# Kernel optimization log

Hardware: AMD Instinct MI355X
Metric: run time of the kernel (lower is better)

Reference implementation:

```python
import jax, jax.numpy as jnp
import numpy as np

N = 100000
E = 3200000
F_IN = 27
H1, C1 = 8, 8
H2, C2 = 1, 2
NEG_SLOPE = 0.2


def gat_conv(x, src, dst, W, a_src, a_dst, b, heads, ch, n_nodes):
    # x: [N, F_in]; src/dst: [E'] (self-loops already appended)
    h = (x @ W).reshape(n_nodes, heads, ch)            # [N, H, C]
    alpha_src = jnp.sum(h * a_src, axis=-1)            # [N, H]
    alpha_dst = jnp.sum(h * a_dst, axis=-1)            # [N, H]
    e = jax.nn.leaky_relu(alpha_src[src] + alpha_dst[dst], NEG_SLOPE)  # [E', H]
    m = jax.ops.segment_max(e, dst, num_segments=n_nodes)             # [N, H]
    ex = jnp.exp(e - m[dst])
    denom = jax.ops.segment_sum(ex, dst, num_segments=n_nodes)        # [N, H]
    alpha = ex / denom[dst]                                           # [E', H]
    out = jax.ops.segment_sum(h[src] * alpha[:, :, None], dst, num_segments=n_nodes)
    return out.reshape(n_nodes, heads * ch) + b


def setup_inputs() -> dict:
    key = jax.random.key(0)
    ks = jax.random.split(key, 10)
    x = jax.random.normal(ks[0], (N, F_IN), dtype=jnp.float32)
    edge_index = jax.random.randint(ks[1], (2, E), 0, N, dtype=jnp.int64)
    s1 = 1.0 / np.sqrt(F_IN)
    s2 = 1.0 / np.sqrt(H1 * C1)
    W1 = jax.random.uniform(ks[2], (F_IN, H1 * C1), jnp.float32, -s1, s1)
    a_src1 = jax.random.uniform(ks[3], (H1, C1), jnp.float32, -s1, s1)
    a_dst1 = jax.random.uniform(ks[4], (H1, C1), jnp.float32, -s1, s1)
    b1 = jnp.zeros((H1 * C1,), jnp.float32)
    W2 = jax.random.uniform(ks[5], (H1 * C1, H2 * C2), jnp.float32, -s2, s2)
    a_src2 = jax.random.uniform(ks[6], (H2, C2), jnp.float32, -s2, s2)
    a_dst2 = jax.random.uniform(ks[7], (H2, C2), jnp.float32, -s2, s2)
    b2 = jnp.zeros((H2 * C2,), jnp.float32)
    return {"x": x, "edge_index": edge_index, "W1": W1, "a_src1": a_src1,
            "a_dst1": a_dst1, "b1": b1, "W2": W2, "a_src2": a_src2,
            "a_dst2": a_dst2, "b2": b2}


def reference(x, edge_index, W1, a_src1, a_dst1, b1, W2, a_src2, a_dst2, b2):
    # eval mode: dropouts are identity. PyG GATConv adds self-loops by default.
    loop = jnp.arange(N, dtype=edge_index.dtype)
    src = jnp.concatenate([edge_index[0], loop])
    dst = jnp.concatenate([edge_index[1], loop])
    h = jax.nn.elu(gat_conv(x, src, dst, W1, a_src1, a_dst1, b1, H1, C1, N))
    out = gat_conv(h, src, dst, W2, a_src2, a_dst2, b2, H2, C2, N)
    return jax.nn.log_softmax(out, axis=1)
```

## Files before the change

kernel.cpp:

```cpp
#include <hip/hip_runtime.h>
#include <hip/hip_fp16.h>
#include <math.h>

#define NN 100000
#define EE 3200000
#define ET (EE + NN)

#define H1n 8
#define C1n 8
#define F1n 64
#define FINn 27
#define NEG 0.2f

#define NPB 128
#define NB 782
#define STRIDE 5120
#define TILE 4096
#define ABLK 256
#define WIN (STRIDE + NPB)

typedef float floatx2 __attribute__((ext_vector_type(2)));

static __device__ __forceinline__ float lrelu(float v) {
    return v > 0.f ? v : NEG * v;
}

__global__ __launch_bounds__(ABLK) void k_binA(const int* __restrict__ ei,
                                               int* __restrict__ tail,
                                               int* __restrict__ recs) {
    __shared__ int hist[NB];
    __shared__ int lofs[NB];
    __shared__ int cur[NB];
    __shared__ int gpos[NB];
    __shared__ int sorted[TILE];
    __shared__ unsigned short sbkt[TILE];
    __shared__ int part[ABLK];

    int tid = threadIdx.x;
    long long e0 = (long long)blockIdx.x * TILE;
    int cnt = (int)min((long long)TILE, (long long)EE - e0);

    for (int i = tid; i < NB; i += ABLK) hist[i] = 0;
    __syncthreads();

    int ss[TILE / ABLK], dd[TILE / ABLK];
    #pragma unroll
    for (int k = 0; k < TILE / ABLK; ++k) {
        int idx = k * ABLK + tid;
        if (idx < cnt) {
            ss[k] = ei[e0 + idx];
            dd[k] = ei[EE + e0 + idx];
            atomicAdd(&hist[dd[k] >> 7], 1);
        }
    }
    __syncthreads();
    {
        const int CH = (NB + ABLK - 1) / ABLK;
        int beg = tid * CH, end = min(beg + CH, NB);
        int s = 0;
        for (int i = beg; i < end; ++i) s += hist[i];
        part[tid] = s;
        __syncthreads();
        for (int off = 1; off < ABLK; off <<= 1) {
            int add = (tid >= off) ? part[tid - off] : 0;
            __syncthreads();
            part[tid] += add;
            __syncthreads();
        }
        int ex = (tid > 0) ? part[tid - 1] : 0;
        for (int i = beg; i < end; ++i) {
            lofs[i] = ex;
            cur[i] = ex;
            ex += hist[i];
        }
    }
    __syncthreads();
    #pragma unroll
    for (int k = 0; k < TILE / ABLK; ++k) {
        int idx = k * ABLK + tid;
        if (idx < cnt) {
            int b = dd[k] >> 7;
            int r = atomicAdd(&cur[b], 1);
            sorted[r] = ss[k] | ((dd[k] & (NPB - 1)) << 17);
            sbkt[r] = (unsigned short)b;
        }
    }
    __syncthreads();
    for (int i = tid; i < NB; i += ABLK) {
        int c = hist[i];
        if (c > 0) gpos[i] = atomicAdd(&tail[i], c);
    }
    __syncthreads();
    for (int t = tid; t < cnt; t += ABLK) {
        int b = sbkt[t];
        recs[(size_t)b * STRIDE + gpos[b] + (t - lofs[b])] = sorted[t];
    }
}

__global__ void k_bscan(const int* __restrict__ tail, int* __restrict__ bbase) {
    __shared__ int part[256];
    int tid = threadIdx.x;
    const int CH = (NB + 255) / 256;
    int beg = tid * CH, end = min(beg + CH, NB);
    int s = 0;
    for (int i = beg; i < end; ++i)
        s += tail[i] + min(NPB, NN - i * NPB);
    part[tid] = s;
    __syncthreads();
    for (int off = 1; off < 256; off <<= 1) {
        int add = (tid >= off) ? part[tid - off] : 0;
        __syncthreads();
        part[tid] += add;
        __syncthreads();
    }
    int ex = (tid > 0) ? part[tid - 1] : 0;
    for (int i = beg; i < end; ++i) {
        bbase[i] = ex;
        ex += tail[i] + min(NPB, NN - i * NPB);
    }
}

__global__ __launch_bounds__(128) void k_binB(const int* __restrict__ recs,
                                              const int* __restrict__ tail,
                                              const int* __restrict__ bbase,
                                              int* __restrict__ rowptr,
                                              int* __restrict__ csr) {
    __shared__ int hist[NPB];
    __shared__ int cur[NPB];
    __shared__ int window[WIN];
    __shared__ int wtot[2];

    int b = blockIdx.x;
    int tid = threadIdx.x;
    int node0 = b * NPB;
    int nodes = min(NPB, NN - node0);
    int cnt = tail[b];
    const int* rb = recs + (size_t)b * STRIDE;

    hist[tid] = 0;
    __syncthreads();
    for (int i = tid; i < cnt; i += 128) atomicAdd(&hist[rb[i] >> 17], 1);
    __syncthreads();
    int v = (tid < nodes) ? hist[tid] + 1 : 0;
    int inc = v;
    #pragma unroll
    for (int off = 1; off < 64; off <<= 1) {
        int t = __shfl_up(inc, off, 64);
        if ((tid & 63) >= off) inc += t;
    }
    if ((tid & 63) == 63) wtot[tid >> 6] = inc;
    __syncthreads();
    if (tid >= 64) inc += wtot[0];
    int T = wtot[0] + wtot[1];
    int ex = inc - v;
    int base = bbase[b];
    if (tid < nodes) {
        rowptr[node0 + tid] = base + ex;
        window[ex] = node0 + tid;
        cur[tid] = ex + 1;
    }
    if (b == NB - 1 && tid == 0) rowptr[NN] = base + T;
    __syncthreads();
    for (int i = tid; i < cnt; i += 128) {
        int r = rb[i];
        int p = atomicAdd(&cur[r >> 17], 1);
        window[p] = r & 0x1FFFF;
    }
    __syncthreads();
    for (int i = tid; i < T; i += 128) csr[base + i] = window[i];
}

__global__ __launch_bounds__(256) void k_h1(const float* __restrict__ x,
                                            const float* __restrict__ W1,
                                            const float* __restrict__ a_src1,
                                            const float* __restrict__ a_dst1,
                                            unsigned char* __restrict__ h1q,
                                            __half* __restrict__ as1h,
                                            float* __restrict__ ad1) {
    int gt = blockIdx.x * blockDim.x + threadIdx.x;
    int n = gt >> 6;
    if (n >= NN) return;
    int lane = threadIdx.x & 63;
    const float* xr = x + (size_t)n * FINn;
    float s = 0.f;
    #pragma unroll
    for (int k = 0; k < FINn; ++k) s = fmaf(xr[k], W1[k * F1n + lane], s);
    float s2 = __shfl_down(s, 1, 64);
    if (!(lane & 1)) {
        int pk = __builtin_amdgcn_cvt_pk_fp8_f32(s, s2, 0, false);
        ((unsigned short*)(h1q + (size_t)n * F1n))[lane >> 1] =
            (unsigned short)(pk & 0xFFFF);
    }
    float ps = s * a_src1[lane];
    float pd = s * a_dst1[lane];
    #pragma unroll
    for (int off = 1; off < 8; off <<= 1) {
        ps += __shfl_xor(ps, off, 64);
        pd += __shfl_xor(pd, off, 64);
    }
    if ((lane & 7) == 0) {
        int h = lane >> 3;
        as1h[n * H1n + h] = __float2half(ps);
        ad1[n * H1n + h] = pd;
    }
}

__global__ __launch_bounds__(256) void k_l1(const int* __restrict__ rowptr,
                                            const int* __restrict__ csr,
                                            const unsigned* __restrict__ h1q,
                                            const __half* __restrict__ as1h,
                                            const float* __restrict__ ad1,
                                            const float* __restrict__ b1,
                                            const float* __restrict__ W2,
                                            const float* __restrict__ a_src2,
                                            const float* __restrict__ a_dst2,
                                            uint2* __restrict__ rec2) {
    int gt = blockIdx.x * blockDim.x + threadIdx.x;
    int n = gt >> 6;
    if (n >= NN) return;
    int lane = threadIdx.x & 63;
    int e8 = lane >> 3;
    int hh = lane & 7;
    int q = lane >> 4;
    int c4 = lane & 15;
    float adh = ad1[(n << 3) + hh];
    int bpe = e8 << 2;
    int bpq = q << 2;
    int bpx = ((q << 3) + (c4 >> 1)) << 2;

    int beg = rowptr[n], end = rowptr[n + 1];
    float a0 = 0.f, a1 = 0.f, a2 = 0.f, a3 = 0.f, den = 0.f;

    for (int base = beg; base < end; base += 64) {
        int cnt = min(64, end - base);
        int sidx = (lane < cnt) ? csr[base + lane] : 0;
        for (int sb = 0; sb < cnt; sb += 8) {
            int sb4 = sb << 2;
            int s_sc = __builtin_amdgcn_ds_bpermute(sb4 + bpe, sidx);
            float A = __half2float(as1h[((unsigned)s_sc << 3) + hh]);
            float sc = A + adh;
            sc = fmaxf(sc, 0.2f * sc);
            float x = (sb + e8 < cnt) ? __expf(sc) : 0.f;
            den += x;
            int xi = __float_as_int(x);
            #pragma unroll
            for (int jj = 0; jj < 2; ++jj) {
                int s_a = __builtin_amdgcn_ds_bpermute(sb4 + (jj << 4) + bpq, sidx);
                int xr_ = __builtin_amdgcn_ds_bpermute((jj << 7) + bpx, xi);
                float xv = __int_as_float(xr_);
                unsigned dw = h1q[((unsigned)s_a << 4) + c4];
                floatx2 lo = __builtin_amdgcn_cvt_pk_f32_fp8((int)dw, false);
                floatx2 hi = __builtin_amdgcn_cvt_pk_f32_fp8((int)dw, true);
                a0 = fmaf(xv, lo.x, a0);
                a1 = fmaf(xv, lo.y, a1);
                a2 = fmaf(xv, hi.x, a2);
                a3 = fmaf(xv, hi.y, a3);
            }
        }
    }

    den += __shfl_xor(den, 8, 64);
    den += __shfl_xor(den, 16, 64);
    den += __shfl_xor(den, 32, 64);
    den = __int_as_float(
        __builtin_amdgcn_ds_bpermute((c4 >> 1) << 2, __float_as_int(den)));
    #pragma unroll
    for (int off = 16; off < 64; off <<= 1) {
        a0 += __shfl_xor(a0, off, 64);
        a1 += __shfl_xor(a1, off, 64);
        a2 += __shfl_xor(a2, off, 64);
        a3 += __shfl_xor(a3, off, 64);
    }
    float inv = 1.f / den;
    float v0 = a0 * inv + b1[c4 * 4 + 0];
    float v1 = a1 * inv + b1[c4 * 4 + 1];
    float v2 = a2 * inv + b1[c4 * 4 + 2];
    float v3 = a3 * inv + b1[c4 * 4 + 3];
    v0 = v0 > 0.f ? v0 : expm1f(v0);
    v1 = v1 > 0.f ? v1 : expm1f(v1);
    v2 = v2 > 0.f ? v2 : expm1f(v2);
    v3 = v3 > 0.f ? v3 : expm1f(v3);
    float p0 = v0 * W2[(c4 * 4 + 0) * 2 + 0] + v1 * W2[(c4 * 4 + 1) * 2 + 0] +
               v2 * W2[(c4 * 4 + 2) * 2 + 0] + v3 * W2[(c4 * 4 + 3) * 2 + 0];
    float p1 = v0 * W2[(c4 * 4 + 0) * 2 + 1] + v1 * W2[(c4 * 4 + 1) * 2 + 1] +
               v2 * W2[(c4 * 4 + 2) * 2 + 1] + v3 * W2[(c4 * 4 + 3) * 2 + 1];
    #pragma unroll
    for (int off = 1; off < 16; off <<= 1) {
        p0 += __shfl_xor(p0, off, 64);
        p1 += __shfl_xor(p1, off, 64);
    }
    if (lane == 0) {
        float as2 = p0 * a_src2[0] + p1 * a_src2[1];
        float ad2 = p0 * a_dst2[0] + p1 * a_dst2[1];
        __half2 lo2 = __floats2half2_rn(p0, p1);
        __half2 hi2 = __floats2half2_rn(as2, ad2);
        uint2 r;
        r.x = *(unsigned*)&lo2;
        r.y = *(unsigned*)&hi2;
        rec2[n] = r;
    }
}

__global__ __launch_bounds__(256) void k_l2(const int* __restrict__ rowptr,
                                            const int* __restrict__ csr,
                                            const uint2* __restrict__ rec2,
                                            const float* __restrict__ b2,
                                            float* __restrict__ out) {
    int gt = blockIdx.x * blockDim.x + threadIdx.x;
    int n = gt >> 6;
    if (n >= NN) return;
    int lane = threadIdx.x & 63;
    __half2 mysd = *(const __half2*)&rec2[n].y;
    float adv = __half2float(__high2half(mysd));
    int beg = rowptr[n], end = rowptr[n + 1];
    float den = 0.f, a0 = 0.f, a1 = 0.f;
    for (int i = beg + lane; i < end; i += 64) {
        int s = csr[i];
        uint2 rv = rec2[s];
        __half2 h01 = *(const __half2*)&rv.x;
        __half2 hsd = *(const __half2*)&rv.y;
        float e = lrelu(__half2float(__low2half(hsd)) + adv);
        float ex = __expf(e);
        den += ex;
        a0 = fmaf(ex, __half2float(__low2half(h01)), a0);
        a1 = fmaf(ex, __half2float(__high2half(h01)), a1);
    }
    #pragma unroll
    for (int off = 32; off > 0; off >>= 1) {
        den += __shfl_xor(den, off, 64);
        a0 += __shfl_xor(a0, off, 64);
        a1 += __shfl_xor(a1, off, 64);
    }
    if (lane == 0) {
        float v0 = a0 / den + b2[0];
        float v1 = a1 / den + b2[1];
        float mx = fmaxf(v0, v1);
        float ls = mx + logf(__expf(v0 - mx) + __expf(v1 - mx));
        out[n * 2 + 0] = v0 - ls;
        out[n * 2 + 1] = v1 - ls;
    }
}

extern "C" void kernel_launch(void* const* d_in, const int* in_sizes, int n_in,
                              void* d_out, int out_size, void* d_ws, size_t ws_size,
                              hipStream_t stream) {
    const float* x      = (const float*)d_in[0];
    const int*   ei     = (const int*)d_in[1];
    const float* W1     = (const float*)d_in[2];
    const float* a_src1 = (const float*)d_in[3];
    const float* a_dst1 = (const float*)d_in[4];
    const float* b1     = (const float*)d_in[5];
    const float* W2     = (const float*)d_in[6];
    const float* a_src2 = (const float*)d_in[7];
    const float* a_dst2 = (const float*)d_in[8];
    const float* b2     = (const float*)d_in[9];
    float* out = (float*)d_out;

    char* wsb = (char*)d_ws;
    size_t o = 0;
    uint2* rec2 = (uint2*)wsb;                   o += (size_t)NN * 8;
    #define ALLOC(name, type, count) type* name = (type*)(wsb + o); o += (size_t)(count) * 4;
    ALLOC(ad1,    float, NN * H1n)
    ALLOC(rowptr, int,   NN + 1)
    ALLOC(csr,    int,   ET)
    ALLOC(recs,   int,   (size_t)NB * STRIDE)
    ALLOC(tail,   int,   NB)
    ALLOC(bbase,  int,   NB)
    #undef ALLOC
    __half* as1h = (__half*)(wsb + o);               o += (size_t)NN * H1n * 2;
    unsigned char* h1q = (unsigned char*)(wsb + o);  o += (size_t)NN * F1n;

    const int B = 256;
    #define GRID(n) ((unsigned)(((long long)(n) + B - 1) / B))

    hipMemsetAsync(tail, 0, (size_t)NB * sizeof(int), stream);
    k_binA<<<(EE + TILE - 1) / TILE, ABLK, 0, stream>>>(ei, tail, recs);
    k_bscan<<<1, 256, 0, stream>>>(tail, bbase);
    k_binB<<<NB, 128, 0, stream>>>(recs, tail, bbase, rowptr, csr);

    k_h1<<<GRID((size_t)NN * 64), B, 0, stream>>>(x, W1, a_src1, a_dst1, h1q, as1h, ad1);

    k_l1<<<GRID((size_t)NN * 64), B, 0, stream>>>(rowptr, csr, (const unsigned*)h1q,
                                                  as1h, ad1, b1, W2, a_src2, a_dst2, rec2);

    k_l2<<<GRID((size_t)NN * 64), B, 0, stream>>>(rowptr, csr, rec2, b2, out);
    #undef GRID
}
```

Measured before the change: 233.6 us.

## Fuse bucket-local CSR build into both GAT aggregation kernels, drop global CSR

Removes the global scan and CSR-building kernels. Each of the two aggregation kernels now rebuilds the per-bucket adjacency of 128 nodes in shared memory from the binned records, then processes those nodes with 8 waves per block. This saves the global CSR and rowptr writes and reads plus two launches. In exchange the bucket-local sort is done twice, the grid shrinks to 782 blocks of 512 threads, and the large shared-memory window may limit occupancy.

```diff
diff --git a/kernel.cpp b/kernel.cpp
--- a/kernel.cpp
+++ b/kernel.cpp
@@ -18,6 +18,7 @@
 #define TILE 4096
 #define ABLK 256
 #define WIN (STRIDE + NPB)
+#define FBLK 512
 
 typedef float floatx2 __attribute__((ext_vector_type(2)));
 
@@ -95,79 +96,6 @@
         int b = sbkt[t];
         recs[(size_t)b * STRIDE + gpos[b] + (t - lofs[b])] = sorted[t];
     }
-}
-
-__global__ void k_bscan(const int* __restrict__ tail, int* __restrict__ bbase) {
-    __shared__ int part[256];
-    int tid = threadIdx.x;
-    const int CH = (NB + 255) / 256;
-    int beg = tid * CH, end = min(beg + CH, NB);
-    int s = 0;
-    for (int i = beg; i < end; ++i)
-        s += tail[i] + min(NPB, NN - i * NPB);
-    part[tid] = s;
-    __syncthreads();
-    for (int off = 1; off < 256; off <<= 1) {
-        int add = (tid >= off) ? part[tid - off] : 0;
-        __syncthreads();
-        part[tid] += add;
-        __syncthreads();
-    }
-    int ex = (tid > 0) ? part[tid - 1] : 0;
-    for (int i = beg; i < end; ++i) {
-        bbase[i] = ex;
-        ex += tail[i] + min(NPB, NN - i * NPB);
-    }
-}
-
-__global__ __launch_bounds__(128) void k_binB(const int* __restrict__ recs,
-                                              const int* __restrict__ tail,
-                                              const int* __restrict__ bbase,
-                                              int* __restrict__ rowptr,
-                                              int* __restrict__ csr) {
-    __shared__ int hist[NPB];
-    __shared__ int cur[NPB];
-    __shared__ int window[WIN];
-    __shared__ int wtot[2];
-
-    int b = blockIdx.x;
-    int tid = threadIdx.x;
-    int node0 = b * NPB;
-    int nodes = min(NPB, NN - node0);
-    int cnt = tail[b];
-    const int* rb = recs + (size_t)b * STRIDE;
-
-    hist[tid] = 0;
-    __syncthreads();
-    for (int i = tid; i < cnt; i += 128) atomicAdd(&hist[rb[i] >> 17], 1);
-    __syncthreads();
-    int v = (tid < nodes) ? hist[tid] + 1 : 0;
-    int inc = v;
-    #pragma unroll
-    for (int off = 1; off < 64; off <<= 1) {
-        int t = __shfl_up(inc, off, 64);
-        if ((tid & 63) >= off) inc += t;
-    }
-    if ((tid & 63) == 63) wtot[tid >> 6] = inc;
-    __syncthreads();
-    if (tid >= 64) inc += wtot[0];
-    int T = wtot[0] + wtot[1];
-    int ex = inc - v;
-    int base = bbase[b];
-    if (tid < nodes) {
-        rowptr[node0 + tid] = base + ex;
-        window[ex] = node0 + tid;
-        cur[tid] = ex + 1;
-    }
-    if (b == NB - 1 && tid == 0) rowptr[NN] = base + T;
-    __syncthreads();
-    for (int i = tid; i < cnt; i += 128) {
-        int r = rb[i];
-        int p = atomicAdd(&cur[r >> 17], 1);
-        window[p] = r & 0x1FFFF;
-    }
-    __syncthreads();
-    for (int i = tid; i < T; i += 128) csr[base + i] = window[i];
 }
 
 __global__ __launch_bounds__(256) void k_h1(const float* __restrict__ x,
@@ -205,139 +133,235 @@
     }
 }
 
-__global__ __launch_bounds__(256) void k_l1(const int* __restrict__ rowptr,
-                                            const int* __restrict__ csr,
-                                            const unsigned* __restrict__ h1q,
-                                            const __half* __restrict__ as1h,
-                                            const float* __restrict__ ad1,
-                                            const float* __restrict__ b1,
-                                            const float* __restrict__ W2,
-                                            const float* __restrict__ a_src2,
-                                            const float* __restrict__ a_dst2,
-                                            uint2* __restrict__ rec2) {
-    int gt = blockIdx.x * blockDim.x + threadIdx.x;
-    int n = gt >> 6;
-    if (n >= NN) return;
-    int lane = threadIdx.x & 63;
+__global__ __launch_bounds__(FBLK) void k_f1(const int* __restrict__ recs,
+                                             const int* __restrict__ tail,
+                                             const unsigned* __restrict__ h1q,
+                                             const __half* __restrict__ as1h,
+                                             const float* __restrict__ ad1,
+                                             const float* __restrict__ b1,
+                                             const float* __restrict__ W2,
+                                             const float* __restrict__ a_src2,
+                                             const float* __restrict__ a_dst2,
+                                             uint2* __restrict__ rec2) {
+    __shared__ int hist[NPB];
+    __shared__ int cur[NPB];
+    __shared__ int rloc[NPB + 1];
+    __shared__ int window[WIN];
+    __shared__ int wtot[2];
+
+    int b = blockIdx.x;
+    int tid = threadIdx.x;
+    int node0 = b * NPB;
+    int nodes = min(NPB, NN - node0);
+    int rcnt = tail[b];
+    const int* rb = recs + (size_t)b * STRIDE;
+
+    if (tid < NPB) hist[tid] = 0;
+    __syncthreads();
+    for (int i = tid; i < rcnt; i += FBLK) atomicAdd(&hist[rb[i] >> 17], 1);
+    __syncthreads();
+    int v = 0, inc = 0;
+    if (tid < NPB) {
+        v = (tid < nodes) ? hist[tid] + 1 : 0;
+        inc = v;
+        #pragma unroll
+        for (int off = 1; off < 64; off <<= 1) {
+            int t = __shfl_up(inc, off, 64);
+            if ((tid & 63) >= off) inc += t;
+        }
+        if ((tid & 63) == 63) wtot[tid >> 6] = inc;
+    }
+    __syncthreads();
+    if (tid < NPB) {
+        if (tid >= 64) inc += wtot[0];
+        int ex = inc - v;
+        if (tid < nodes) {
+            rloc[tid] = ex;
+            cur[tid] = ex + 1;
+            window[ex] = node0 + tid;
+        }
+    }
+    if (tid == 0) rloc[nodes] = wtot[0] + wtot[1];
+    __syncthreads();
+    for (int i = tid; i < rcnt; i += FBLK) {
+        int r = rb[i];
+        int p = atomicAdd(&cur[r >> 17], 1);
+        window[p] = r & 0x1FFFF;
+    }
+    __syncthreads();
+
+    int lane = tid & 63;
+    int wv = tid >> 6;
     int e8 = lane >> 3;
     int hh = lane & 7;
     int q = lane >> 4;
     int c4 = lane & 15;
-    float adh = ad1[(n << 3) + hh];
     int bpe = e8 << 2;
     int bpq = q << 2;
     int bpx = ((q << 3) + (c4 >> 1)) << 2;
 
-    int beg = rowptr[n], end = rowptr[n + 1];
-    float a0 = 0.f, a1 = 0.f, a2 = 0.f, a3 = 0.f, den = 0.f;
-
-    for (int base = beg; base < end; base += 64) {
-        int cnt = min(64, end - base);
-        int sidx = (lane < cnt) ? csr[base + lane] : 0;
-        for (int sb = 0; sb < cnt; sb += 8) {
-            int sb4 = sb << 2;
-            int s_sc = __builtin_amdgcn_ds_bpermute(sb4 + bpe, sidx);
-            float A = __half2float(as1h[((unsigned)s_sc << 3) + hh]);
-            float sc = A + adh;
-            sc = fmaxf(sc, 0.2f * sc);
-            float x = (sb + e8 < cnt) ? __expf(sc) : 0.f;
-            den += x;
-            int xi = __float_as_int(x);
-            #pragma unroll
-            for (int jj = 0; jj < 2; ++jj) {
-                int s_a = __builtin_amdgcn_ds_bpermute(sb4 + (jj << 4) + bpq, sidx);
-                int xr_ = __builtin_amdgcn_ds_bpermute((jj << 7) + bpx, xi);
-                float xv = __int_as_float(xr_);
-                unsigned dw = h1q[((unsigned)s_a << 4) + c4];
-                floatx2 lo = __builtin_amdgcn_cvt_pk_f32_fp8((int)dw, false);
-                floatx2 hi = __builtin_amdgcn_cvt_pk_f32_fp8((int)dw, true);
-                a0 = fmaf(xv, lo.x, a0);
-                a1 = fmaf(xv, lo.y, a1);
-                a2 = fmaf(xv, hi.x, a2);
-                a3 = fmaf(xv, hi.y, a3);
+    for (int ln = wv; ln < nodes; ln += FBLK / 64) {
+        int n = node0 + ln;
+        float adh = ad1[(n << 3) + hh];
+        int beg = rloc[ln], end = rloc[ln + 1];
+        float a0 = 0.f, a1 = 0.f, a2 = 0.f, a3 = 0.f, den = 0.f;
+
+        for (int base = beg; base < end; base += 64) {
+            int cnt = min(64, end - base);
+            int sidx = (lane < cnt) ? window[base + lane] : 0;
+            for (int sb = 0; sb < cnt; sb += 8) {
+                int sb4 = sb << 2;
+                int s_sc = __builtin_amdgcn_ds_bpermute(sb4 + bpe, sidx);
+                float A = __half2float(as1h[((unsigned)s_sc << 3) + hh]);
+                float sc = A + adh;
+                sc = fmaxf(sc, 0.2f * sc);
+                float x = (sb + e8 < cnt) ? __expf(sc) : 0.f;
+                den += x;
+                int xi = __float_as_int(x);
+                #pragma unroll
+                for (int jj = 0; jj < 2; ++jj) {
+                    int s_a = __builtin_amdgcn_ds_bpermute(sb4 + (jj << 4) + bpq, sidx);
+                    int xr_ = __builtin_amdgcn_ds_bpermute((jj << 7) + bpx, xi);
+                    float xv = __int_as_float(xr_);
+                    unsigned dw = h1q[((unsigned)s_a << 4) + c4];
+                    floatx2 lo = __builtin_amdgcn_cvt_pk_f32_fp8((int)dw, false);
+                    floatx2 hi = __builtin_amdgcn_cvt_pk_f32_fp8((int)dw, true);
+                    a0 = fmaf(xv, lo.x, a0);
+                    a1 = fmaf(xv, lo.y, a1);
+                    a2 = fmaf(xv, hi.x, a2);
+                    a3 = fmaf(xv, hi.y, a3);
+                }
             }
         }
-    }
-
-    den += __shfl_xor(den, 8, 64);
-    den += __shfl_xor(den, 16, 64);
-    den += __shfl_xor(den, 32, 64);
-    den = __int_as_float(
-        __builtin_amdgcn_ds_bpermute((c4 >> 1) << 2, __float_as_int(den)));
-    #pragma unroll
-    for (int off = 16; off < 64; off <<= 1) {
-        a0 += __shfl_xor(a0, off, 64);
-        a1 += __shfl_xor(a1, off, 64);
-        a2 += __shfl_xor(a2, off, 64);
-        a3 += __shfl_xor(a3, off, 64);
-    }
-    float inv = 1.f / den;
-    float v0 = a0 * inv + b1[c4 * 4 + 0];
-    float v1 = a1 * inv + b1[c4 * 4 + 1];
-    float v2 = a2 * inv + b1[c4 * 4 + 2];
-    float v3 = a3 * inv + b1[c4 * 4 + 3];
-    v0 = v0 > 0.f ? v0 : expm1f(v0);
-    v1 = v1 > 0.f ? v1 : expm1f(v1);
-    v2 = v2 > 0.f ? v2 : expm1f(v2);
-    v3 = v3 > 0.f ? v3 : expm1f(v3);
-    float p0 = v0 * W2[(c4 * 4 + 0) * 2 + 0] + v1 * W2[(c4 * 4 + 1) * 2 + 0] +
-               v2 * W2[(c4 * 4 + 2) * 2 + 0] + v3 * W2[(c4 * 4 + 3) * 2 + 0];
-    float p1 = v0 * W2[(c4 * 4 + 0) * 2 + 1] + v1 * W2[(c4 * 4 + 1) * 2 + 1] +
-               v2 * W2[(c4 * 4 + 2) * 2 + 1] + v3 * W2[(c4 * 4 + 3) * 2 + 1];
-    #pragma unroll
-    for (int off = 1; off < 16; off <<= 1) {
-        p0 += __shfl_xor(p0, off, 64);
-        p1 += __shfl_xor(p1, off, 64);
-    }
-    if (lane == 0) {
-        float as2 = p0 * a_src2[0] + p1 * a_src2[1];
-        float ad2 = p0 * a_dst2[0] + p1 * a_dst2[1];
-        __half2 lo2 = __floats2half2_rn(p0, p1);
-        __half2 hi2 = __floats2half2_rn(as2, ad2);
-        uint2 r;
-        r.x = *(unsigned*)&lo2;
-        r.y = *(unsigned*)&hi2;
-        rec2[n] = r;
-    }
-}
-
-__global__ __launch_bounds__(256) void k_l2(const int* __restrict__ rowptr,
-                                            const int* __restrict__ csr,
-                                            const uint2* __restrict__ rec2,
-                                            const float* __restrict__ b2,
-                                            float* __restrict__ out) {
-    int gt = blockIdx.x * blockDim.x + threadIdx.x;
-    int n = gt >> 6;
-    if (n >= NN) return;
-    int lane = threadIdx.x & 63;
-    __half2 mysd = *(const __half2*)&rec2[n].y;
-    float adv = __half2float(__high2half(mysd));
-    int beg = rowptr[n], end = rowptr[n + 1];
-    float den = 0.f, a0 = 0.f, a1 = 0.f;
-    for (int i = beg + lane; i < end; i += 64) {
-        int s = csr[i];
-        uint2 rv = rec2[s];
-        __half2 h01 = *(const __half2*)&rv.x;
-        __half2 hsd = *(const __half2*)&rv.y;
-        float e = lrelu(__half2float(__low2half(hsd)) + adv);
-        float ex = __expf(e);
-        den += ex;
-        a0 = fmaf(ex, __half2float(__low2half(h01)), a0);
-        a1 = fmaf(ex, __half2float(__high2half(h01)), a1);
-    }
-    #pragma unroll
-    for (int off = 32; off > 0; off >>= 1) {
-        den += __shfl_xor(den, off, 64);
-        a0 += __shfl_xor(a0, off, 64);
-        a1 += __shfl_xor(a1, off, 64);
-    }
-    if (lane == 0) {
-        float v0 = a0 / den + b2[0];
-        float v1 = a1 / den + b2[1];
-        float mx = fmaxf(v0, v1);
-        float ls = mx + logf(__expf(v0 - mx) + __expf(v1 - mx));
-        out[n * 2 + 0] = v0 - ls;
-        out[n * 2 + 1] = v1 - ls;
+
+        den += __shfl_xor(den, 8, 64);
+        den += __shfl_xor(den, 16, 64);
+        den += __shfl_xor(den, 32, 64);
+        den = __int_as_float(
+            __builtin_amdgcn_ds_bpermute((c4 >> 1) << 2, __float_as_int(den)));
+        #pragma unroll
+        for (int off = 16; off < 64; off <<= 1) {
+            a0 += __shfl_xor(a0, off, 64);
+            a1 += __shfl_xor(a1, off, 64);
+            a2 += __shfl_xor(a2, off, 64);
+            a3 += __shfl_xor(a3, off, 64);
+        }
+        float inv = 1.f / den;
+        float v0 = a0 * inv + b1[c4 * 4 + 0];
+        float v1 = a1 * inv + b1[c4 * 4 + 1];
+        float v2 = a2 * inv + b1[c4 * 4 + 2];
+        float v3 = a3 * inv + b1[c4 * 4 + 3];
+        v0 = v0 > 0.f ? v0 : expm1f(v0);
+        v1 = v1 > 0.f ? v1 : expm1f(v1);
+        v2 = v2 > 0.f ? v2 : expm1f(v2);
+        v3 = v3 > 0.f ? v3 : expm1f(v3);
+        float p0 = v0 * W2[(c4 * 4 + 0) * 2 + 0] + v1 * W2[(c4 * 4 + 1) * 2 + 0] +
+                   v2 * W2[(c4 * 4 + 2) * 2 + 0] + v3 * W2[(c4 * 4 + 3) * 2 + 0];
+        float p1 = v0 * W2[(c4 * 4 + 0) * 2 + 1] + v1 * W2[(c4 * 4 + 1) * 2 + 1] +
+                   v2 * W2[(c4 * 4 + 2) * 2 + 1] + v3 * W2[(c4 * 4 + 3) * 2 + 1];
+        #pragma unroll
+        for (int off = 1; off < 16; off <<= 1) {
+            p0 += __shfl_xor(p0, off, 64);
+            p1 += __shfl_xor(p1, off, 64);
+        }
+        if (lane == 0) {
+            float as2 = p0 * a_src2[0] + p1 * a_src2[1];
+            float ad2 = p0 * a_dst2[0] + p1 * a_dst2[1];
+            __half2 lo2 = __floats2half2_rn(p0, p1);
+            __half2 hi2 = __floats2half2_rn(as2, ad2);
+            uint2 r;
+            r.x = *(unsigned*)&lo2;
+            r.y = *(unsigned*)&hi2;
+            rec2[n] = r;
+        }
+    }
+}
+
+__global__ __launch_bounds__(FBLK) void k_f2(const int* __restrict__ recs,
+                                             const int* __restrict__ tail,
+                                             const uint2* __restrict__ rec2,
+                                             const float* __restrict__ b2,
+                                             float* __restrict__ out) {
+    __shared__ int hist[NPB];
+    __shared__ int cur[NPB];
+    __shared__ int rloc[NPB + 1];
+    __shared__ int window[WIN];
+    __shared__ int wtot[2];
+
+    int b = blockIdx.x;
+    int tid = threadIdx.x;
+    int node0 = b * NPB;
+    int nodes = min(NPB, NN - node0);
+    int rcnt = tail[b];
+    const int* rb = recs + (size_t)b * STRIDE;
+
+    if (tid < NPB) hist[tid] = 0;
+    __syncthreads();
+    for (int i = tid; i < rcnt; i += FBLK) atomicAdd(&hist[rb[i] >> 17], 1);
+    __syncthreads();
+    int v = 0, inc = 0;
+    if (tid < NPB) {
+        v = (tid < nodes) ? hist[tid] + 1 : 0;
+        inc = v;
+        #pragma unroll
+        for (int off = 1; off < 64; off <<= 1) {
+            int t = __shfl_up(inc, off, 64);
+            if ((tid & 63) >= off) inc += t;
+        }
+        if ((tid & 63) == 63) wtot[tid >> 6] = inc;
+    }
+    __syncthreads();
+    if (tid < NPB) {
+        if (tid >= 64) inc += wtot[0];
+        int ex = inc - v;
+        if (tid < nodes) {
+            rloc[tid] = ex;
+            cur[tid] = ex + 1;
+            window[ex] = node0 + tid;
+        }
+    }
+    if (tid == 0) rloc[nodes] = wtot[0] + wtot[1];
+    __syncthreads();
+    for (int i = tid; i < rcnt; i += FBLK) {
+        int r = rb[i];
+        int p = atomicAdd(&cur[r >> 17], 1);
+        window[p] = r & 0x1FFFF;
+    }
+    __syncthreads();
+
+    int lane = tid & 63;
+    int wv = tid >> 6;
+    for (int ln = wv; ln < nodes; ln += FBLK / 64) {
+        int n = node0 + ln;
+        __half2 mysd = *(const __half2*)&rec2[n].y;
+        float adv = __half2float(__high2half(mysd));
+        int beg = rloc[ln], end = rloc[ln + 1];
+        float den = 0.f, a0 = 0.f, a1 = 0.f;
+        for (int i = beg + lane; i < end; i += 64) {
+            int s = window[i];
+            uint2 rv = rec2[s];
+            __half2 h01 = *(const __half2*)&rv.x;
+            __half2 hsd = *(const __half2*)&rv.y;
+            float e = lrelu(__half2float(__low2half(hsd)) + adv);
+            float ex = __expf(e);
+            den += ex;
+            a0 = fmaf(ex, __half2float(__low2half(h01)), a0);
+            a1 = fmaf(ex, __half2float(__high2half(h01)), a1);
+        }
+        #pragma unroll
+        for (int off = 32; off > 0; off >>= 1) {
+            den += __shfl_xor(den, off, 64);
+            a0 += __shfl_xor(a0, off, 64);
+            a1 += __shfl_xor(a1, off, 64);
+        }
+        if (lane == 0) {
+            float v0 = a0 / den + b2[0];
+            float v1 = a1 / den + b2[1];
+            float mx = fmaxf(v0, v1);
+            float ls = mx + logf(__expf(v0 - mx) + __expf(v1 - mx));
+            out[n * 2 + 0] = v0 - ls;
+            out[n * 2 + 1] = v1 - ls;
+        }
     }
 }
 
@@ -361,11 +385,8 @@
     uint2* rec2 = (uint2*)wsb;                   o += (size_t)NN * 8;
     #define ALLOC(name, type, count) type* name = (type*)(wsb + o); o += (size_t)(count) * 4;
     ALLOC(ad1,    float, NN * H1n)
-    ALLOC(rowptr, int,   NN + 1)
-    ALLOC(csr,    int,   ET)
     ALLOC(recs,   int,   (size_t)NB * STRIDE)
     ALLOC(tail,   int,   NB)
-    ALLOC(bbase,  int,   NB)
     #undef ALLOC
     __half* as1h = (__half*)(wsb + o);               o += (size_t)NN * H1n * 2;
     unsigned char* h1q = (unsigned char*)(wsb + o);  o += (size_t)NN * F1n;
@@ -375,14 +396,12 @@
 
     hipMemsetAsync(tail, 0, (size_t)NB * sizeof(int), stream);
     k_binA<<<(EE + TILE - 1) / TILE, ABLK, 0, stream>>>(ei, tail, recs);
-    k_bscan<<<1, 256, 0, stream>>>(tail, bbase);
-    k_binB<<<NB, 128, 0, stream>>>(recs, tail, bbase, rowptr, csr);
 
     k_h1<<<GRID((size_t)NN * 64), B, 0, stream>>>(x, W1, a_src1, a_dst1, h1q, as1h, ad1);
 
-    k_l1<<<GRID((size_t)NN * 64), B, 0, stream>>>(rowptr, csr, (const unsigned*)h1q,
-                                                  as1h, ad1, b1, W2, a_src2, a_dst2, rec2);
-
-    k_l2<<<GRID((size_t)NN * 64), B, 0, stream>>>(rowptr, csr, rec2, b2, out);
+    k_f1<<<NB, FBLK, 0, stream>>>(recs, tail, (const unsigned*)h1q, as1h, ad1, b1,
+                                  W2, a_src2, a_dst2, rec2);
+
+    k_f2<<<NB, FBLK, 0, stream>>>(recs, tail, rec2, b2, out);
     #undef GRID
 }
```

Result: faster. 218.2 us (-6.6%).
